# Performance work log

Measured on AMD Instinct MI355X. Metric: run time of the kernel, lower is better.

The kernel has to match this reference:

```python
import jax, jax.numpy as jnp
import numpy as np

B, T, IN, H, OUT = 512, 2048, 16, 128, 8


def setup_inputs() -> dict:
    key = jax.random.key(0)
    ks = jax.random.split(key, 12)
    s = 0.05
    return {
        "x": jax.random.normal(ks[0], (B, T, IN), dtype=jnp.float32),
        "W_ih0": jax.random.normal(ks[1], (3 * H, IN), dtype=jnp.float32) * s,
        "W_hh0": jax.random.normal(ks[2], (3 * H, H), dtype=jnp.float32) * s,
        "b_ih0": jax.random.normal(ks[3], (3 * H,), dtype=jnp.float32) * s,
        "b_hh0": jax.random.normal(ks[4], (3 * H,), dtype=jnp.float32) * s,
        "W_ih1": jax.random.normal(ks[5], (3 * H, H), dtype=jnp.float32) * s,
        "W_hh1": jax.random.normal(ks[6], (3 * H, H), dtype=jnp.float32) * s,
        "b_ih1": jax.random.normal(ks[7], (3 * H,), dtype=jnp.float32) * s,
        "b_hh1": jax.random.normal(ks[8], (3 * H,), dtype=jnp.float32) * s,
        "W_out": jax.random.normal(ks[9], (OUT, H), dtype=jnp.float32) * s,
        "b_out": jax.random.normal(ks[10], (OUT,), dtype=jnp.float32) * s,
    }


def _gru_cell(xg, h, W_hh, b_hh):
    # xg: precomputed x @ W_ih.T + b_ih, shape [B, 3H]; PyTorch gate order r,z,n
    hg = h @ W_hh.T + b_hh
    xr, xz, xn = jnp.split(xg, 3, axis=-1)
    hr, hz, hn = jnp.split(hg, 3, axis=-1)
    r = jax.nn.sigmoid(xr + hr)
    z = jax.nn.sigmoid(xz + hz)
    n = jnp.tanh(xn + r * hn)
    return (1.0 - z) * n + z * h


def reference(x, W_ih0, W_hh0, b_ih0, b_hh0, W_ih1, W_hh1, b_ih1, b_hh1, W_out, b_out):
    # Precompute layer-0 input gates for all timesteps: [T, B, 3H]
    xg0 = jnp.einsum('bti,gi->tbg', x, W_ih0) + b_ih0

    def step(carry, xg_t):
        h0, h1 = carry
        h0 = _gru_cell(xg_t, h0, W_hh0, b_hh0)
        xg1 = h0 @ W_ih1.T + b_ih1
        h1 = _gru_cell(xg1, h1, W_hh1, b_hh1)
        return (h0, h1), h1

    h0 = jnp.zeros((x.shape[0], W_hh0.shape[1]), dtype=x.dtype)
    h1 = jnp.zeros((x.shape[0], W_hh1.shape[1]), dtype=x.dtype)
    _, h1_seq = jax.lax.scan(step, (h0, h1), xg0)  # [T, B, H]
    out = jnp.einsum('tbh,oh->bto', h1_seq, W_out) + b_out  # [B, T, OUT]
    return out
```

## Files before the change

### kernel.cpp

```cpp
#include <hip/hip_runtime.h>


typedef unsigned int uint;
typedef _Float16 v8h __attribute__((ext_vector_type(8)));
typedef float    v4f __attribute__((ext_vector_type(4)));

#define Tq   2048
#define INq  16
#define Hq   128
#define OUTq 8
#define BW   16

#define MFMA(a,b,c) __builtin_amdgcn_mfma_f32_16x16x32_f16((a),(b),(c),0,0,0)

__device__ __forceinline__ float sigm(float x){
  return __builtin_amdgcn_rcpf(1.0f + __expf(-x));
}
__device__ __forceinline__ float tanh_f(float x){
  return 1.0f - 2.0f*__builtin_amdgcn_rcpf(__expf(2.0f*x) + 1.0f);
}
__device__ __forceinline__ int achunk(int row, int kq){
  return row*4 + (kq ^ ((row>>1)&3));
}

__global__ __launch_bounds__(512,2) void gru2_kernel(
    const float* __restrict__ x,
    const float* __restrict__ Wih0, const float* __restrict__ Whh0,
    const float* __restrict__ bih0, const float* __restrict__ bhh0,
    const float* __restrict__ Wih1, const float* __restrict__ Whh1,
    const float* __restrict__ bih1, const float* __restrict__ bhh1,
    const float* __restrict__ Wout, const float* __restrict__ bout,
    float* __restrict__ out)
{
  const int tid  = threadIdx.x;
  const int lane = tid & 63;
  const int w    = tid >> 6;
  const int col  = lane & 15;
  const int bg   = lane >> 4;
  const int b0   = blockIdx.x * BW;
  const int hb   = 16*w + col;

  const float* xrow = &x[(size_t)(b0+col)*Tq*INq];
  float4 xfa, xfb;
  if (bg < 2){
    xfa = *(const float4*)&xrow[0*INq + bg*8 + 0];
    xfb = *(const float4*)&xrow[0*INq + bg*8 + 4];
  }

  __shared__ __align__(16) _Float16 hA0[2][2048];
  __shared__ __align__(16) _Float16 hA1[2][2048];

  for (int i=tid; i<2048; i+=512) ((uint*)hA0)[i] = 0u;
  for (int i=tid; i<2048; i+=512) ((uint*)hA1)[i] = 0u;

  v8h Fhh0[3][4], Fih1[3][4], Fhh1[3][4], Fx[3], Fo[4];
  #pragma unroll
  for (int g=0; g<3; ++g){
    const int r = g*Hq + hb;
    #pragma unroll
    for (int ks=0; ks<4; ++ks){
      const float* p0 = &Whh0[r*Hq + ks*32 + bg*8];
      const float* p1 = &Wih1[r*Hq + ks*32 + bg*8];
      const float* p2 = &Whh1[r*Hq + ks*32 + bg*8];
      v8h a, b, c;
      #pragma unroll
      for (int e=0;e<8;++e){ a[e]=(_Float16)p0[e]; b[e]=(_Float16)p1[e]; c[e]=(_Float16)p2[e]; }
      Fhh0[g][ks]=a; Fih1[g][ks]=b; Fhh1[g][ks]=c;
    }
    v8h vx;
    #pragma unroll
    for (int e=0;e<8;++e) vx[e]=(_Float16)0.f;
    if (bg < 2){
      const float* p = &Wih0[r*INq + bg*8];
      #pragma unroll
      for (int e=0;e<8;++e) vx[e]=(_Float16)p[e];
    }
    Fx[g]=vx;
  }
  #pragma unroll
  for (int ks=0; ks<4; ++ks){
    v8h v;
    #pragma unroll
    for (int e=0;e<8;++e) v[e]=(_Float16)0.f;
    if (col < OUTq){
      const float* p = &Wout[col*Hq + ks*32 + bg*8];
      #pragma unroll
      for (int e=0;e<8;++e) v[e]=(_Float16)p[e];
    }
    Fo[ks]=v;
  }
  const float bo_s  = (col<OUTq) ? bout[col] : 0.f;
  const float bs_r  = bih0[hb]      + bhh0[hb];
  const float bs_z  = bih0[Hq+hb]   + bhh0[Hq+hb];
  const float bs_nx = bih0[2*Hq+hb];
  const float bs_nh = bhh0[2*Hq+hb];
  const float c1_r  = bih1[hb]      + bhh1[hb];
  const float c1_z  = bih1[Hq+hb]   + bhh1[Hq+hb];
  const float c1_nx = bih1[2*Hq+hb];
  const float c1_nh = bhh1[2*Hq+hb];

  float h0s[4] = {0,0,0,0};
  float h1s[4] = {0,0,0,0};

  const int rch    = achunk(col, bg);
  const int wtile  = hb >> 5;
  const int kq_w   = (hb >> 3) & 3;
  const int elem_w = hb & 7;

  __syncthreads();

  for (int t=0; t<Tq; ++t){
    const int cur = t & 1, prv = cur ^ 1;

    v8h ax;
    #pragma unroll
    for (int e=0;e<8;++e) ax[e]=(_Float16)0.f;
    if (bg < 2){
      ax[0]=(_Float16)xfa.x; ax[1]=(_Float16)xfa.y; ax[2]=(_Float16)xfa.z; ax[3]=(_Float16)xfa.w;
      ax[4]=(_Float16)xfb.x; ax[5]=(_Float16)xfb.y; ax[6]=(_Float16)xfb.z; ax[7]=(_Float16)xfb.w;
    }

    v4f aR  = {bs_r, bs_r, bs_r, bs_r};
    v4f aZ  = {bs_z, bs_z, bs_z, bs_z};
    v4f aNX = {bs_nx,bs_nx,bs_nx,bs_nx};
    v4f aNH = {bs_nh,bs_nh,bs_nh,bs_nh};
    aR  = MFMA(ax, Fx[0], aR);
    aZ  = MFMA(ax, Fx[1], aZ);
    aNX = MFMA(ax, Fx[2], aNX);
    #pragma unroll
    for (int ks=0;ks<4;++ks){
      v8h a = *(const v8h*)&hA0[prv][ks*512 + rch*8];
      aR  = MFMA(a, Fhh0[0][ks], aR);
      aZ  = MFMA(a, Fhh0[1][ks], aZ);
      aNH = MFMA(a, Fhh0[2][ks], aNH);
    }
    const bool doout = ((t&1)==0) && (t>=2) && (w<2);
    v4f ao;
    if (doout){
      const _Float16* hsrc = (w==0) ? &hA1[cur][0] : &hA1[prv][0];
      ao = (v4f){0.f,0.f,0.f,0.f};
      #pragma unroll
      for (int ks=0;ks<4;++ks){
        v8h a = *(const v8h*)&hsrc[ks*512 + rch*8];
        ao = MFMA(a, Fo[ks], ao);
      }
    }
    #pragma unroll
    for (int j=0;j<4;++j){
      float r = sigm(aR[j]);
      float z = sigm(aZ[j]);
      float n = tanh_f(aNX[j] + r*aNH[j]);
      float h = n + z*(h0s[j]-n);
      h0s[j]=h;
      hA0[cur][wtile*512 + achunk(bg*4+j, kq_w)*8 + elem_w] = (_Float16)h;
    }
    __syncthreads();

    if (doout && col < OUTq){
      const int to = t - 2 + w;
      #pragma unroll
      for (int j=0;j<4;++j)
        out[(size_t)((b0 + bg*4 + j)*Tq + to)*OUTq + col] = ao[j] + bo_s;
    }
    if (bg < 2){
      const int tn = (t+1 < Tq) ? t+1 : Tq-1;
      xfa = *(const float4*)&xrow[tn*INq + bg*8 + 0];
      xfb = *(const float4*)&xrow[tn*INq + bg*8 + 4];
    }

    v4f cR  = {c1_r, c1_r, c1_r, c1_r};
    v4f cZ  = {c1_z, c1_z, c1_z, c1_z};
    v4f cNX = {c1_nx,c1_nx,c1_nx,c1_nx};
    v4f cNH = {c1_nh,c1_nh,c1_nh,c1_nh};
    #pragma unroll
    for (int ks=0;ks<4;++ks){
      v8h a0 = *(const v8h*)&hA0[cur][ks*512 + rch*8];
      v8h a1 = *(const v8h*)&hA1[prv][ks*512 + rch*8];
      cR  = MFMA(a0, Fih1[0][ks], cR);
      cZ  = MFMA(a0, Fih1[1][ks], cZ);
      cNX = MFMA(a0, Fih1[2][ks], cNX);
      cR  = MFMA(a1, Fhh1[0][ks], cR);
      cZ  = MFMA(a1, Fhh1[1][ks], cZ);
      cNH = MFMA(a1, Fhh1[2][ks], cNH);
    }
    #pragma unroll
    for (int j=0;j<4;++j){
      float r = sigm(cR[j]);
      float z = sigm(cZ[j]);
      float n = tanh_f(cNX[j] + r*cNH[j]);
      float h = n + z*(h1s[j]-n);
      h1s[j]=h;
      hA1[cur][wtile*512 + achunk(bg*4+j, kq_w)*8 + elem_w] = (_Float16)h;
    }
    __syncthreads();
  }

  if (w < 2){
    const _Float16* hsrc = &hA1[w][0];
    v4f ao = {0.f,0.f,0.f,0.f};
    #pragma unroll
    for (int ks=0;ks<4;++ks){
      v8h a = *(const v8h*)&hsrc[ks*512 + rch*8];
      ao = MFMA(a, Fo[ks], ao);
    }
    if (col < OUTq){
      const int to = Tq - 2 + w;
      #pragma unroll
      for (int j=0;j<4;++j)
        out[(size_t)((b0 + bg*4 + j)*Tq + to)*OUTq + col] = ao[j] + bo_s;
    }
  }
}

extern "C" void kernel_launch(void* const* d_in, const int* in_sizes, int n_in,
                              void* d_out, int out_size, void* d_ws, size_t ws_size,
                              hipStream_t stream) {
  const float* x    = (const float*)d_in[0];
  const float* Wih0 = (const float*)d_in[1];
  const float* Whh0 = (const float*)d_in[2];
  const float* bih0 = (const float*)d_in[3];
  const float* bhh0 = (const float*)d_in[4];
  const float* Wih1 = (const float*)d_in[5];
  const float* Whh1 = (const float*)d_in[6];
  const float* bih1 = (const float*)d_in[7];
  const float* bhh1 = (const float*)d_in[8];
  const float* Wout = (const float*)d_in[9];
  const float* bo   = (const float*)d_in[10];
  gru2_kernel<<<dim3(32), dim3(512), 0, stream>>>(
      x, Wih0, Whh0, bih0, bhh0, Wih1, Whh1, bih1, bhh1, Wout, bo,
      (float*)d_out);
}
```

Measured before the change: 3.056 ms.

## Transpose MFMA operands, pack hidden-state LDS stores, move output projection to one wave

Swaps the MFMA operand order so the weights become the A operand and the hidden state the B operand. Each lane now holds four consecutive hidden units and writes them to shared memory as one packed 8-byte store with a new XOR swizzle, instead of four scalar half stores. The output projection moves from waves 0-1 every other step to wave 7 every step, placed in the layer-1 phase. Barriers become a raw s_barrier with an explicit lgkmcnt wait, and the next x prefetch is hoisted ahead of the layer-0 MFMAs. The aim is to cut LDS store count, barrier overhead and load imbalance on the serial per-step critical path, at the cost of extra work on wave 7.

```diff
diff --git a/kernel.cpp b/kernel.cpp
--- a/kernel.cpp
+++ b/kernel.cpp
@@ -1,9 +1,11 @@
 #include <hip/hip_runtime.h>
 
 
-typedef unsigned int uint;
+typedef unsigned int  uint;
+typedef unsigned short ushort;
 typedef _Float16 v8h __attribute__((ext_vector_type(8)));
 typedef float    v4f __attribute__((ext_vector_type(4)));
+typedef uint     v2u __attribute__((ext_vector_type(2)));
 
 #define Tq   2048
 #define INq  16
@@ -12,6 +14,9 @@
 #define BW   16
 
 #define MFMA(a,b,c) __builtin_amdgcn_mfma_f32_16x16x32_f16((a),(b),(c),0,0,0)
+#define BAR() do { asm volatile("s_waitcnt lgkmcnt(0)" ::: "memory"); \
+                   __builtin_amdgcn_s_barrier(); \
+                   asm volatile("" ::: "memory"); } while(0)
 
 __device__ __forceinline__ float sigm(float x){
   return __builtin_amdgcn_rcpf(1.0f + __expf(-x));
@@ -19,8 +24,12 @@
 __device__ __forceinline__ float tanh_f(float x){
   return 1.0f - 2.0f*__builtin_amdgcn_rcpf(__expf(2.0f*x) + 1.0f);
 }
-__device__ __forceinline__ int achunk(int row, int kq){
-  return row*4 + (kq ^ ((row>>1)&3));
+__device__ __forceinline__ uint packh2(float lo, float hi){
+  _Float16 a=(_Float16)lo, b=(_Float16)hi;
+  return (uint)__builtin_bit_cast(ushort,a) | ((uint)__builtin_bit_cast(ushort,b)<<16);
+}
+__device__ __forceinline__ v4f ld4(const float* p){
+  return *reinterpret_cast<const v4f*>(p);
 }
 
 __global__ __launch_bounds__(512,2) void gru2_kernel(
@@ -35,23 +44,21 @@
   const int tid  = threadIdx.x;
   const int lane = tid & 63;
   const int w    = tid >> 6;
-  const int col  = lane & 15;
+  const int nb   = lane & 15;
   const int bg   = lane >> 4;
   const int b0   = blockIdx.x * BW;
-  const int hb   = 16*w + col;
-
-  const float* xrow = &x[(size_t)(b0+col)*Tq*INq];
+  const int hb   = 16*w + nb;
+
+  __shared__ __align__(16) _Float16 hA0[2][2048];
+  __shared__ __align__(16) _Float16 hA1[2][2048];
+  for (int i=tid; i<2048; i+=512){ ((uint*)hA0)[i]=0u; ((uint*)hA1)[i]=0u; }
+
+  const float* xrow = x + (size_t)(b0+nb)*Tq*INq;
   float4 xfa, xfb;
   if (bg < 2){
-    xfa = *(const float4*)&xrow[0*INq + bg*8 + 0];
-    xfb = *(const float4*)&xrow[0*INq + bg*8 + 4];
-  }
-
-  __shared__ __align__(16) _Float16 hA0[2][2048];
-  __shared__ __align__(16) _Float16 hA1[2][2048];
-
-  for (int i=tid; i<2048; i+=512) ((uint*)hA0)[i] = 0u;
-  for (int i=tid; i<2048; i+=512) ((uint*)hA1)[i] = 0u;
+    xfa = *(const float4*)(xrow + 0*INq + bg*8);
+    xfb = *(const float4*)(xrow + 0*INq + bg*8 + 4);
+  }
 
   v8h Fhh0[3][4], Fih1[3][4], Fhh1[3][4], Fx[3], Fo[4];
   #pragma unroll
@@ -82,35 +89,38 @@
     v8h v;
     #pragma unroll
     for (int e=0;e<8;++e) v[e]=(_Float16)0.f;
-    if (col < OUTq){
-      const float* p = &Wout[col*Hq + ks*32 + bg*8];
+    if (nb < OUTq){
+      const float* p = &Wout[nb*Hq + ks*32 + bg*8];
       #pragma unroll
       for (int e=0;e<8;++e) v[e]=(_Float16)p[e];
     }
     Fo[ks]=v;
   }
-  const float bo_s  = (col<OUTq) ? bout[col] : 0.f;
-  const float bs_r  = bih0[hb]      + bhh0[hb];
-  const float bs_z  = bih0[Hq+hb]   + bhh0[Hq+hb];
-  const float bs_nx = bih0[2*Hq+hb];
-  const float bs_nh = bhh0[2*Hq+hb];
-  const float c1_r  = bih1[hb]      + bhh1[hb];
-  const float c1_z  = bih1[Hq+hb]   + bhh1[Hq+hb];
-  const float c1_nx = bih1[2*Hq+hb];
-  const float c1_nh = bhh1[2*Hq+hb];
+
+  const int hb4 = 16*w + bg*4;
+  const v4f bR4  = ld4(bih0+hb4)      + ld4(bhh0+hb4);
+  const v4f bZ4  = ld4(bih0+Hq+hb4)   + ld4(bhh0+Hq+hb4);
+  const v4f bNX4 = ld4(bih0+2*Hq+hb4);
+  const v4f bNH4 = ld4(bhh0+2*Hq+hb4);
+  const v4f cR4  = ld4(bih1+hb4)      + ld4(bhh1+hb4);
+  const v4f cZ4  = ld4(bih1+Hq+hb4)   + ld4(bhh1+Hq+hb4);
+  const v4f cNX4 = ld4(bih1+2*Hq+hb4);
+  const v4f cNH4 = ld4(bhh1+2*Hq+hb4);
+  v4f bo4 = {0.f,0.f,0.f,0.f};
+  if (bg < 2) bo4 = ld4(bout + bg*4);
 
   float h0s[4] = {0,0,0,0};
   float h1s[4] = {0,0,0,0};
 
-  const int rch    = achunk(col, bg);
-  const int wtile  = hb >> 5;
-  const int kq_w   = (hb >> 3) & 3;
-  const int elem_w = hb & 7;
+  int rb[4];
+  #pragma unroll
+  for (int ks=0; ks<4; ++ks) rb[ks] = nb*128 + (((ks*4+bg) ^ nb))*8;
+  const int wof = nb*128 + (((2*w + (bg>>1)) ^ nb))*8 + (bg&1)*4;
 
   __syncthreads();
 
   for (int t=0; t<Tq; ++t){
-    const int cur = t & 1, prv = cur ^ 1;
+    const int cur = t&1, prv = cur^1;
 
     v8h ax;
     #pragma unroll
@@ -120,94 +130,85 @@
       ax[4]=(_Float16)xfb.x; ax[5]=(_Float16)xfb.y; ax[6]=(_Float16)xfb.z; ax[7]=(_Float16)xfb.w;
     }
 
-    v4f aR  = {bs_r, bs_r, bs_r, bs_r};
-    v4f aZ  = {bs_z, bs_z, bs_z, bs_z};
-    v4f aNX = {bs_nx,bs_nx,bs_nx,bs_nx};
-    v4f aNH = {bs_nh,bs_nh,bs_nh,bs_nh};
-    aR  = MFMA(ax, Fx[0], aR);
-    aZ  = MFMA(ax, Fx[1], aZ);
-    aNX = MFMA(ax, Fx[2], aNX);
-    #pragma unroll
-    for (int ks=0;ks<4;++ks){
-      v8h a = *(const v8h*)&hA0[prv][ks*512 + rch*8];
-      aR  = MFMA(a, Fhh0[0][ks], aR);
-      aZ  = MFMA(a, Fhh0[1][ks], aZ);
-      aNH = MFMA(a, Fhh0[2][ks], aNH);
-    }
-    const bool doout = ((t&1)==0) && (t>=2) && (w<2);
-    v4f ao;
-    if (doout){
-      const _Float16* hsrc = (w==0) ? &hA1[cur][0] : &hA1[prv][0];
-      ao = (v4f){0.f,0.f,0.f,0.f};
-      #pragma unroll
-      for (int ks=0;ks<4;++ks){
-        v8h a = *(const v8h*)&hsrc[ks*512 + rch*8];
-        ao = MFMA(a, Fo[ks], ao);
-      }
-    }
+    v4f aR=bR4, aZ=bZ4, aNX=bNX4, aNH=bNH4;
+    aR  = MFMA(Fx[0], ax, aR);
+    aZ  = MFMA(Fx[1], ax, aZ);
+    aNX = MFMA(Fx[2], ax, aNX);
+    if (bg < 2){
+      const int tn = (t+1 < Tq) ? t+1 : Tq-1;
+      xfa = *(const float4*)(xrow + tn*INq + bg*8);
+      xfb = *(const float4*)(xrow + tn*INq + bg*8 + 4);
+    }
+    #pragma unroll
+    for (int ks=0; ks<4; ++ks){
+      v8h a = *(const v8h*)&hA0[prv][rb[ks]];
+      aR  = MFMA(Fhh0[0][ks], a, aR);
+      aZ  = MFMA(Fhh0[1][ks], a, aZ);
+      aNH = MFMA(Fhh0[2][ks], a, aNH);
+    }
+    float hn0[4];
     #pragma unroll
     for (int j=0;j<4;++j){
       float r = sigm(aR[j]);
       float z = sigm(aZ[j]);
       float n = tanh_f(aNX[j] + r*aNH[j]);
       float h = n + z*(h0s[j]-n);
-      h0s[j]=h;
-      hA0[cur][wtile*512 + achunk(bg*4+j, kq_w)*8 + elem_w] = (_Float16)h;
-    }
-    __syncthreads();
-
-    if (doout && col < OUTq){
-      const int to = t - 2 + w;
-      #pragma unroll
-      for (int j=0;j<4;++j)
-        out[(size_t)((b0 + bg*4 + j)*Tq + to)*OUTq + col] = ao[j] + bo_s;
-    }
-    if (bg < 2){
-      const int tn = (t+1 < Tq) ? t+1 : Tq-1;
-      xfa = *(const float4*)&xrow[tn*INq + bg*8 + 0];
-      xfb = *(const float4*)&xrow[tn*INq + bg*8 + 4];
-    }
-
-    v4f cR  = {c1_r, c1_r, c1_r, c1_r};
-    v4f cZ  = {c1_z, c1_z, c1_z, c1_z};
-    v4f cNX = {c1_nx,c1_nx,c1_nx,c1_nx};
-    v4f cNH = {c1_nh,c1_nh,c1_nh,c1_nh};
-    #pragma unroll
-    for (int ks=0;ks<4;++ks){
-      v8h a0 = *(const v8h*)&hA0[cur][ks*512 + rch*8];
-      v8h a1 = *(const v8h*)&hA1[prv][ks*512 + rch*8];
-      cR  = MFMA(a0, Fih1[0][ks], cR);
-      cZ  = MFMA(a0, Fih1[1][ks], cZ);
-      cNX = MFMA(a0, Fih1[2][ks], cNX);
-      cR  = MFMA(a1, Fhh1[0][ks], cR);
-      cZ  = MFMA(a1, Fhh1[1][ks], cZ);
-      cNH = MFMA(a1, Fhh1[2][ks], cNH);
-    }
+      h0s[j]=h; hn0[j]=h;
+    }
+    { v2u pk; pk[0]=packh2(hn0[0],hn0[1]); pk[1]=packh2(hn0[2],hn0[3]);
+      *(v2u*)&hA0[cur][wof] = pk; }
+    BAR();
+
+    v4f cR=cR4, cZ=cZ4, cNX=cNX4, cNH=cNH4;
+    #pragma unroll
+    for (int ks=0; ks<4; ++ks){
+      v8h a0 = *(const v8h*)&hA0[cur][rb[ks]];
+      v8h a1 = *(const v8h*)&hA1[prv][rb[ks]];
+      cR  = MFMA(Fih1[0][ks], a0, cR);
+      cZ  = MFMA(Fih1[1][ks], a0, cZ);
+      cNX = MFMA(Fih1[2][ks], a0, cNX);
+      cR  = MFMA(Fhh1[0][ks], a1, cR);
+      cZ  = MFMA(Fhh1[1][ks], a1, cZ);
+      cNH = MFMA(Fhh1[2][ks], a1, cNH);
+    }
+    if (w == 7){
+      v4f oac = {0.f,0.f,0.f,0.f};
+      #pragma unroll
+      for (int ks=0; ks<4; ++ks){
+        v8h a1 = *(const v8h*)&hA1[prv][rb[ks]];
+        oac = MFMA(Fo[ks], a1, oac);
+      }
+      if (t > 0 && bg < 2){
+        float4 o;
+        o.x=oac[0]+bo4[0]; o.y=oac[1]+bo4[1]; o.z=oac[2]+bo4[2]; o.w=oac[3]+bo4[3];
+        *(float4*)&out[((size_t)(b0+nb)*Tq + (t-1))*OUTq + bg*4] = o;
+      }
+    }
+    float hn1[4];
     #pragma unroll
     for (int j=0;j<4;++j){
       float r = sigm(cR[j]);
       float z = sigm(cZ[j]);
       float n = tanh_f(cNX[j] + r*cNH[j]);
       float h = n + z*(h1s[j]-n);
-      h1s[j]=h;
-      hA1[cur][wtile*512 + achunk(bg*4+j, kq_w)*8 + elem_w] = (_Float16)h;
-    }
-    __syncthreads();
-  }
-
-  if (w < 2){
-    const _Float16* hsrc = &hA1[w][0];
-    v4f ao = {0.f,0.f,0.f,0.f};
-    #pragma unroll
-    for (int ks=0;ks<4;++ks){
-      v8h a = *(const v8h*)&hsrc[ks*512 + rch*8];
-      ao = MFMA(a, Fo[ks], ao);
-    }
-    if (col < OUTq){
-      const int to = Tq - 2 + w;
-      #pragma unroll
-      for (int j=0;j<4;++j)
-        out[(size_t)((b0 + bg*4 + j)*Tq + to)*OUTq + col] = ao[j] + bo_s;
+      h1s[j]=h; hn1[j]=h;
+    }
+    { v2u pk; pk[0]=packh2(hn1[0],hn1[1]); pk[1]=packh2(hn1[2],hn1[3]);
+      *(v2u*)&hA1[cur][wof] = pk; }
+    BAR();
+  }
+
+  if (w == 7){
+    v4f oac = {0.f,0.f,0.f,0.f};
+    #pragma unroll
+    for (int ks=0; ks<4; ++ks){
+      v8h a1 = *(const v8h*)&hA1[1][rb[ks]];
+      oac = MFMA(Fo[ks], a1, oac);
+    }
+    if (bg < 2){
+      float4 o;
+      o.x=oac[0]+bo4[0]; o.y=oac[1]+bo4[1]; o.z=oac[2]+bo4[2]; o.w=oac[3]+bo4[3];
+      *(float4*)&out[((size_t)(b0+nb)*Tq + (Tq-1))*OUTq + bg*4] = o;
     }
   }
 }
```

Result: slower. 3.296 ms (+7.9%).

## Hoist layer-1 recurrent MFMAs before the first barrier and reuse loaded h tiles

Applied to the files above, without the earlier changes.

Each step now loads the previous hA0 and hA1 fragments up front and computes the layer-1 W_hh contribution before the layer-0 barrier, so only the W_ih1 part stays on the critical path after the sync. The output projection moves to a single wave (w==7) every step and reuses the already-loaded hA1 fragments, instead of two waves every other step doing their own LDS reads. The next x prefetch is issued earlier in the step. This shortens the dependent chain between the two barriers, at the cost of more live registers and a heavier workload on wave 7.

```diff
diff --git a/kernel.cpp b/kernel.cpp
--- a/kernel.cpp
+++ b/kernel.cpp
@@ -1,7 +1,8 @@
 #include <hip/hip_runtime.h>
 
 
-typedef unsigned int uint;
+typedef unsigned int  uint;
+typedef unsigned short ushort;
 typedef _Float16 v8h __attribute__((ext_vector_type(8)));
 typedef float    v4f __attribute__((ext_vector_type(4)));
 
@@ -18,6 +19,10 @@
 }
 __device__ __forceinline__ float tanh_f(float x){
   return 1.0f - 2.0f*__builtin_amdgcn_rcpf(__expf(2.0f*x) + 1.0f);
+}
+__device__ __forceinline__ uint packh2(float lo, float hi){
+  _Float16 a=(_Float16)lo, b=(_Float16)hi;
+  return (uint)__builtin_bit_cast(ushort,a) | ((uint)__builtin_bit_cast(ushort,b)<<16);
 }
 __device__ __forceinline__ int achunk(int row, int kq){
   return row*4 + (kq ^ ((row>>1)&3));
@@ -50,8 +55,7 @@
   __shared__ __align__(16) _Float16 hA0[2][2048];
   __shared__ __align__(16) _Float16 hA1[2][2048];
 
-  for (int i=tid; i<2048; i+=512) ((uint*)hA0)[i] = 0u;
-  for (int i=tid; i<2048; i+=512) ((uint*)hA1)[i] = 0u;
+  for (int i = tid; i < 2048; i += 512){ ((uint*)hA0)[i]=0u; ((uint*)hA1)[i]=0u; }
 
   v8h Fhh0[3][4], Fih1[3][4], Fhh1[3][4], Fx[3], Fo[4];
   #pragma unroll
@@ -112,12 +116,22 @@
   for (int t=0; t<Tq; ++t){
     const int cur = t & 1, prv = cur ^ 1;
 
+    v8h a0k[4], a1k[4];
+    #pragma unroll
+    for (int ks=0; ks<4; ++ks){
+      a0k[ks] = *(const v8h*)&hA0[prv][ks*512 + rch*8];
+      a1k[ks] = *(const v8h*)&hA1[prv][ks*512 + rch*8];
+    }
+
     v8h ax;
     #pragma unroll
     for (int e=0;e<8;++e) ax[e]=(_Float16)0.f;
     if (bg < 2){
       ax[0]=(_Float16)xfa.x; ax[1]=(_Float16)xfa.y; ax[2]=(_Float16)xfa.z; ax[3]=(_Float16)xfa.w;
       ax[4]=(_Float16)xfb.x; ax[5]=(_Float16)xfb.y; ax[6]=(_Float16)xfb.z; ax[7]=(_Float16)xfb.w;
+      int tn = t+1; if (tn > Tq-1) tn = Tq-1;
+      xfa = *(const float4*)&xrow[tn*INq + bg*8 + 0];
+      xfb = *(const float4*)&xrow[tn*INq + bg*8 + 4];
     }
 
     v4f aR  = {bs_r, bs_r, bs_r, bs_r};
@@ -128,86 +142,78 @@
     aZ  = MFMA(ax, Fx[1], aZ);
     aNX = MFMA(ax, Fx[2], aNX);
     #pragma unroll
-    for (int ks=0;ks<4;++ks){
-      v8h a = *(const v8h*)&hA0[prv][ks*512 + rch*8];
-      aR  = MFMA(a, Fhh0[0][ks], aR);
-      aZ  = MFMA(a, Fhh0[1][ks], aZ);
-      aNH = MFMA(a, Fhh0[2][ks], aNH);
-    }
-    const bool doout = ((t&1)==0) && (t>=2) && (w<2);
-    v4f ao;
-    if (doout){
-      const _Float16* hsrc = (w==0) ? &hA1[cur][0] : &hA1[prv][0];
-      ao = (v4f){0.f,0.f,0.f,0.f};
-      #pragma unroll
-      for (int ks=0;ks<4;++ks){
-        v8h a = *(const v8h*)&hsrc[ks*512 + rch*8];
-        ao = MFMA(a, Fo[ks], ao);
-      }
-    }
+    for (int ks=0; ks<4; ++ks){
+      aR  = MFMA(a0k[ks], Fhh0[0][ks], aR);
+      aZ  = MFMA(a0k[ks], Fhh0[1][ks], aZ);
+      aNH = MFMA(a0k[ks], Fhh0[2][ks], aNH);
+    }
+    v4f cR  = {c1_r, c1_r, c1_r, c1_r};
+    v4f cZ  = {c1_z, c1_z, c1_z, c1_z};
+    v4f cNH = {c1_nh,c1_nh,c1_nh,c1_nh};
+    #pragma unroll
+    for (int ks=0; ks<4; ++ks){
+      cR  = MFMA(a1k[ks], Fhh1[0][ks], cR);
+      cZ  = MFMA(a1k[ks], Fhh1[1][ks], cZ);
+      cNH = MFMA(a1k[ks], Fhh1[2][ks], cNH);
+    }
+    v4f oac = {0.f,0.f,0.f,0.f};
+    if (w == 7){
+      #pragma unroll
+      for (int ks=0; ks<4; ++ks) oac = MFMA(a1k[ks], Fo[ks], oac);
+    }
+    float hn0[4];
     #pragma unroll
     for (int j=0;j<4;++j){
       float r = sigm(aR[j]);
       float z = sigm(aZ[j]);
       float n = tanh_f(aNX[j] + r*aNH[j]);
       float h = n + z*(h0s[j]-n);
-      h0s[j]=h;
-      hA0[cur][wtile*512 + achunk(bg*4+j, kq_w)*8 + elem_w] = (_Float16)h;
-    }
+      h0s[j]=h; hn0[j]=h;
+    }
+    #pragma unroll
+    for (int j=0;j<4;++j)
+      hA0[cur][wtile*512 + achunk(bg*4+j, kq_w)*8 + elem_w] = (_Float16)hn0[j];
     __syncthreads();
 
-    if (doout && col < OUTq){
-      const int to = t - 2 + w;
+    if (w == 7 && t > 0 && col < OUTq){
       #pragma unroll
       for (int j=0;j<4;++j)
-        out[(size_t)((b0 + bg*4 + j)*Tq + to)*OUTq + col] = ao[j] + bo_s;
-    }
-    if (bg < 2){
-      const int tn = (t+1 < Tq) ? t+1 : Tq-1;
-      xfa = *(const float4*)&xrow[tn*INq + bg*8 + 0];
-      xfb = *(const float4*)&xrow[tn*INq + bg*8 + 4];
-    }
-
-    v4f cR  = {c1_r, c1_r, c1_r, c1_r};
-    v4f cZ  = {c1_z, c1_z, c1_z, c1_z};
+        out[(size_t)((b0 + bg*4 + j)*Tq + (t-1))*OUTq + col] = oac[j] + bo_s;
+    }
     v4f cNX = {c1_nx,c1_nx,c1_nx,c1_nx};
-    v4f cNH = {c1_nh,c1_nh,c1_nh,c1_nh};
-    #pragma unroll
-    for (int ks=0;ks<4;++ks){
-      v8h a0 = *(const v8h*)&hA0[cur][ks*512 + rch*8];
-      v8h a1 = *(const v8h*)&hA1[prv][ks*512 + rch*8];
-      cR  = MFMA(a0, Fih1[0][ks], cR);
-      cZ  = MFMA(a0, Fih1[1][ks], cZ);
-      cNX = MFMA(a0, Fih1[2][ks], cNX);
-      cR  = MFMA(a1, Fhh1[0][ks], cR);
-      cZ  = MFMA(a1, Fhh1[1][ks], cZ);
-      cNH = MFMA(a1, Fhh1[2][ks], cNH);
-    }
+    #pragma unroll
+    for (int ks=0; ks<4; ++ks){
+      v8h a0n = *(const v8h*)&hA0[cur][ks*512 + rch*8];
+      cR  = MFMA(a0n, Fih1[0][ks], cR);
+      cZ  = MFMA(a0n, Fih1[1][ks], cZ);
+      cNX = MFMA(a0n, Fih1[2][ks], cNX);
+    }
+    float hn1[4];
     #pragma unroll
     for (int j=0;j<4;++j){
       float r = sigm(cR[j]);
       float z = sigm(cZ[j]);
       float n = tanh_f(cNX[j] + r*cNH[j]);
       float h = n + z*(h1s[j]-n);
-      h1s[j]=h;
-      hA1[cur][wtile*512 + achunk(bg*4+j, kq_w)*8 + elem_w] = (_Float16)h;
-    }
+      h1s[j]=h; hn1[j]=h;
+    }
+    #pragma unroll
+    for (int j=0;j<4;++j)
+      hA1[cur][wtile*512 + achunk(bg*4+j, kq_w)*8 + elem_w] = (_Float16)hn1[j];
     __syncthreads();
   }
 
-  if (w < 2){
-    const _Float16* hsrc = &hA1[w][0];
-    v4f ao = {0.f,0.f,0.f,0.f};
-    #pragma unroll
-    for (int ks=0;ks<4;++ks){
-      v8h a = *(const v8h*)&hsrc[ks*512 + rch*8];
-      ao = MFMA(a, Fo[ks], ao);
+  if (w == 7){
+    v4f oac = {0.f,0.f,0.f,0.f};
+    #pragma unroll
+    for (int ks=0; ks<4; ++ks){
+      v8h a1 = *(const v8h*)&hA1[1][ks*512 + rch*8];
+      oac = MFMA(a1, Fo[ks], oac);
     }
     if (col < OUTq){
-      const int to = Tq - 2 + w;
       #pragma unroll
       for (int j=0;j<4;++j)
-        out[(size_t)((b0 + bg*4 + j)*Tq + to)*OUTq + col] = ao[j] + bo_s;
+        out[(size_t)((b0 + bg*4 + j)*Tq + (Tq-1))*OUTq + col] = oac[j] + bo_s;
     }
   }
 }
```

Measured after the change: 7.518 ms. 2.46x slower.
